# Optimization experiments

Measured on AMD Instinct MI355X. Metric: run time of the kernel, lower is better.

Reference implementation:

```python
import jax, jax.numpy as jnp
import numpy as np

B, S, E, H = 4, 2048, 1024, 16
DH = E // H  # 64
DF = 4 * E   # 4096
EPS = 1e-5


def layer_norm(x, g, b):
    mu = jnp.mean(x, axis=-1, keepdims=True)
    var = jnp.mean(jnp.square(x - mu), axis=-1, keepdims=True)
    return (x - mu) * jax.lax.rsqrt(var + EPS) * g + b


def setup_inputs() -> dict:
    key = jax.random.key(0)
    ks = jax.random.split(key, 16)
    s_e = 1.0 / np.sqrt(E)
    s_f = 1.0 / np.sqrt(DF)
    inp = {
        "x": jax.random.normal(ks[0], (B, S, E), jnp.float32),
        # per-head projections stacked over heads: [H, E, DH]
        "wq": jax.random.normal(ks[1], (H, E, DH), jnp.float32) * s_e,
        "wk": jax.random.normal(ks[2], (H, E, DH), jnp.float32) * s_e,
        "wv": jax.random.normal(ks[3], (H, E, DH), jnp.float32) * s_e,
        # output projection [H*DH, E] with bias
        "wo": jax.random.normal(ks[4], (H * DH, E), jnp.float32) * s_e,
        "bo": jax.random.normal(ks[5], (E,), jnp.float32) * 0.01,
        # SwiGLU FFN
        "w1": jax.random.normal(ks[6], (E, DF), jnp.float32) * s_e,
        "b1": jax.random.normal(ks[7], (DF,), jnp.float32) * 0.01,
        "w2": jax.random.normal(ks[8], (E, DF), jnp.float32) * s_e,
        "b2": jax.random.normal(ks[9], (DF,), jnp.float32) * 0.01,
        "w3": jax.random.normal(ks[10], (DF, E), jnp.float32) * s_f,
        "b3": jax.random.normal(ks[11], (E,), jnp.float32) * 0.01,
        # LayerNorm params
        "g1": jnp.ones((E,), jnp.float32),
        "be1": jnp.zeros((E,), jnp.float32),
        "g2": jnp.ones((E,), jnp.float32),
        "be2": jnp.zeros((E,), jnp.float32),
    }
    return inp


def reference(x, wq, wk, wv, wo, bo, w1, b1, w2, b2, w3, b3, g1, be1, g2, be2):
    # --- LN1 + multi-head causal attention ---
    h = layer_norm(x, g1, be1)                       # [B,S,E]
    q = jnp.einsum('bse,hed->bhsd', h, wq)           # [B,H,S,DH]
    k = jnp.einsum('bse,hed->bhsd', h, wk)
    v = jnp.einsum('bse,hed->bhsd', h, wv)
    scores = jnp.einsum('bhsd,bhtd->bhst', q, k) * (DH ** -0.5)  # [B,H,S,S]
    causal = jnp.tril(jnp.ones((S, S), bool))
    scores = jnp.where(causal, scores, -jnp.inf)
    attn = jax.nn.softmax(scores, axis=-1)
    ctx = jnp.einsum('bhst,bhtd->bhsd', attn, v)     # [B,H,S,DH]
    ctx = ctx.transpose(0, 2, 1, 3).reshape(B, S, H * DH)  # concat heads
    attn_out = ctx @ wo + bo                         # [B,S,E]
    r1 = x + attn_out
    # --- LN2 + SwiGLU FFN ---
    h2 = layer_norm(r1, g2, be2)
    a = h2 @ w1 + b1                                 # [B,S,DF]
    gate = h2 @ w2 + b2
    ff = (a * jax.nn.sigmoid(a) * gate) @ w3 + b3    # [B,S,E]
    return r1 + ff
```

## Files before the change

kernel.cpp:

```cpp
#include <hip/hip_runtime.h>
#include <hip/hip_bf16.h>
#include <cstdint>


typedef __bf16 bf16_t;
typedef __attribute__((ext_vector_type(8))) __bf16 bf16x8;
typedef __attribute__((ext_vector_type(4))) __bf16 bf16x4;
typedef __attribute__((ext_vector_type(4))) float f32x4;

#define LOG2E 1.4426950408889634f

static __device__ __forceinline__ void gll16(const void* g, void* l) {
  __builtin_amdgcn_global_load_lds(
      (const __attribute__((address_space(1))) void*)g,
      (__attribute__((address_space(3))) void*)l, 16, 0, 0);
}

__global__ __launch_bounds__(256)
void transpose_cvt(const float* __restrict__ in, bf16_t* __restrict__ out,
                   int R, int C, long in_batch, long out_batch)
{
  __shared__ float tile[64][65];
  const float* inp = in + (long)blockIdx.z * in_batch;
  bf16_t* outp = out + (long)blockIdx.z * out_batch;
  const int c0 = blockIdx.x * 64, r0 = blockIdx.y * 64;
  for (int rr = threadIdx.y; rr < 64; rr += 4)
    tile[rr][threadIdx.x] = inp[(long)(r0 + rr) * C + c0 + threadIdx.x];
  __syncthreads();
  for (int cc = threadIdx.y; cc < 64; cc += 4)
    outp[(long)(c0 + cc) * R + r0 + threadIdx.x] = (bf16_t)tile[threadIdx.x][cc];
}

__global__ __launch_bounds__(256)
void ln_kernel(const float* __restrict__ x, const float* __restrict__ g,
               const float* __restrict__ be, bf16_t* __restrict__ out)
{
  const long row = blockIdx.x;
  const float4 v = ((const float4*)(x + row * 1024))[threadIdx.x];
  float s  = v.x + v.y + v.z + v.w;
  float s2 = v.x*v.x + v.y*v.y + v.z*v.z + v.w*v.w;
  #pragma unroll
  for (int m = 1; m < 64; m <<= 1) {
    s  += __shfl_xor(s, m, 64);
    s2 += __shfl_xor(s2, m, 64);
  }
  __shared__ float red[8];
  const int w = threadIdx.x >> 6, lane = threadIdx.x & 63;
  if (lane == 0) { red[w] = s; red[4 + w] = s2; }
  __syncthreads();
  s  = red[0] + red[1] + red[2] + red[3];
  s2 = red[4] + red[5] + red[6] + red[7];
  const float mu = s * (1.f / 1024.f);
  const float rs = rsqrtf(s2 * (1.f / 1024.f) - mu * mu + 1e-5f);
  const int c = threadIdx.x * 4;
  bf16x4 o;
  o[0] = (bf16_t)((v.x - mu) * rs * g[c+0] + be[c+0]);
  o[1] = (bf16_t)((v.y - mu) * rs * g[c+1] + be[c+1]);
  o[2] = (bf16_t)((v.z - mu) * rs * g[c+2] + be[c+2]);
  o[3] = (bf16_t)((v.w - mu) * rs * g[c+3] + be[c+3]);
  *(bf16x4*)(out + row * 1024 + c) = o;
}

template<int EPI>
__global__ __launch_bounds__(256)
void gemm16(const bf16_t* __restrict__ A, const bf16_t* __restrict__ Bt,
            const float* __restrict__ bias, const float* __restrict__ res,
            float* __restrict__ outF,
            bf16_t* __restrict__ outQ, bf16_t* __restrict__ outK, bf16_t* __restrict__ outV,
            int M, int N, int K)
{
  __shared__ __align__(16) bf16_t As[2][128 * 32];
  __shared__ __align__(16) bf16_t Bs[2][128 * 32];
  const int tid = threadIdx.x, lane = tid & 63, w = tid >> 6;
  const int wr = w >> 1, wc = w & 1;
  const long row0 = (long)blockIdx.y * 128;
  const long col0 = (long)blockIdx.x * 128;
  const int rsub = lane >> 2;
  const int csub = (lane & 3) * 8;
  f32x4 acc[4][4] = {};

  auto stage = [&](long k0, int buf) {
    #pragma unroll
    for (int i = 0; i < 2; ++i) {
      const int c = i * 4 + w;
      gll16(A  + (row0 + c * 16 + rsub) * (long)K + k0 + csub, (char*)As[buf] + c * 1024);
      gll16(Bt + (col0 + c * 16 + rsub) * (long)K + k0 + csub, (char*)Bs[buf] + c * 1024);
    }
  };

  stage(0, 0);
  __syncthreads();
  int cur = 0;
  for (long k0 = 0; k0 < K; k0 += 32) {
    if (k0 + 32 < K) stage(k0 + 32, cur ^ 1);
    const int kof = (lane >> 4) * 8;
    bf16x8 af[4], bfr[4];
    #pragma unroll
    for (int m = 0; m < 4; ++m)
      af[m] = *(const bf16x8*)(As[cur] + (wr * 64 + m * 16 + (lane & 15)) * 32 + kof);
    #pragma unroll
    for (int n = 0; n < 4; ++n)
      bfr[n] = *(const bf16x8*)(Bs[cur] + (wc * 64 + n * 16 + (lane & 15)) * 32 + kof);
    #pragma unroll
    for (int m = 0; m < 4; ++m)
      #pragma unroll
      for (int n = 0; n < 4; ++n)
        acc[m][n] = __builtin_amdgcn_mfma_f32_16x16x32_bf16(af[m], bfr[n], acc[m][n], 0, 0, 0);
    __syncthreads();
    cur ^= 1;
  }
  #pragma unroll
  for (int m = 0; m < 4; ++m) {
    #pragma unroll
    for (int n = 0; n < 4; ++n) {
      const long cc = col0 + wc * 64 + n * 16 + (lane & 15);
      #pragma unroll
      for (int r = 0; r < 4; ++r) {
        const long rr = row0 + wr * 64 + m * 16 + (lane >> 4) * 4 + r;
        const float v = acc[m][n][r];
        if constexpr (EPI == 0) {
          const int which = (int)(cc >> 10);
          const int hh = (int)((cc >> 6) & 15);
          const int d  = (int)(cc & 63);
          const long b = rr >> 11, s = rr & 2047;
          const bf16_t bv = (bf16_t)v;
          const long bh = b * 16 + hh;
          if (which == 0)      outQ[(bh * 2048 + s) * 64 + d] = bv;
          else if (which == 1) outK[(bh * 2048 + s) * 64 + d] = bv;
          else                 outV[(bh * 64 + d) * 2048 + s] = bv;
        } else {
          outF[rr * N + cc] = v + bias[cc] + res[rr * N + cc];
        }
      }
    }
  }
}

__global__ __launch_bounds__(256)
void gemm_dual(const bf16_t* __restrict__ A,
               const bf16_t* __restrict__ B1t, const bf16_t* __restrict__ B2t,
               const float* __restrict__ bias1, const float* __restrict__ bias2,
               bf16_t* __restrict__ out, int M, int N, int K)
{
  __shared__ __align__(16) bf16_t As[2][128 * 32];
  __shared__ __align__(16) bf16_t B1s[2][64 * 32];
  __shared__ __align__(16) bf16_t B2s[2][64 * 32];
  const int tid = threadIdx.x, lane = tid & 63, w = tid >> 6;
  const int wr = w >> 1, wc = w & 1;
  const long row0 = (long)blockIdx.y * 128;
  const long col0 = (long)blockIdx.x * 64;
  const int rsub = lane >> 2;
  const int csub = (lane & 3) * 8;
  const int l15 = lane & 15;
  f32x4 acc1[4][2] = {}, acc2[4][2] = {};

  auto stage = [&](long k0, int buf) {
    gll16(A   + (row0 + w * 16       + rsub) * (long)K + k0 + csub, (char*)As[buf]  + w * 1024);
    gll16(A   + (row0 + (w + 4) * 16 + rsub) * (long)K + k0 + csub, (char*)As[buf]  + (w + 4) * 1024);
    gll16(B1t + (col0 + w * 16       + rsub) * (long)K + k0 + csub, (char*)B1s[buf] + w * 1024);
    gll16(B2t + (col0 + w * 16       + rsub) * (long)K + k0 + csub, (char*)B2s[buf] + w * 1024);
  };

  stage(0, 0);
  __syncthreads();
  int cur = 0;
  for (long k0 = 0; k0 < K; k0 += 32) {
    if (k0 + 32 < K) stage(k0 + 32, cur ^ 1);
    const int kof = (lane >> 4) * 8;
    bf16x8 af[4], b1f[2], b2f[2];
    #pragma unroll
    for (int m = 0; m < 4; ++m)
      af[m] = *(const bf16x8*)(As[cur] + (wr * 64 + m * 16 + l15) * 32 + kof);
    #pragma unroll
    for (int n = 0; n < 2; ++n) {
      b1f[n] = *(const bf16x8*)(B1s[cur] + (wc * 32 + n * 16 + l15) * 32 + kof);
      b2f[n] = *(const bf16x8*)(B2s[cur] + (wc * 32 + n * 16 + l15) * 32 + kof);
    }
    #pragma unroll
    for (int m = 0; m < 4; ++m)
      #pragma unroll
      for (int n = 0; n < 2; ++n) {
        acc1[m][n] = __builtin_amdgcn_mfma_f32_16x16x32_bf16(af[m], b1f[n], acc1[m][n], 0, 0, 0);
        acc2[m][n] = __builtin_amdgcn_mfma_f32_16x16x32_bf16(af[m], b2f[n], acc2[m][n], 0, 0, 0);
      }
    __syncthreads();
    cur ^= 1;
  }
  #pragma unroll
  for (int m = 0; m < 4; ++m) {
    #pragma unroll
    for (int n = 0; n < 2; ++n) {
      const long cc = col0 + wc * 32 + n * 16 + l15;
      #pragma unroll
      for (int r = 0; r < 4; ++r) {
        const long rr = row0 + wr * 64 + m * 16 + (lane >> 4) * 4 + r;
        const float a = acc1[m][n][r] + bias1[cc];
        const float gt = acc2[m][n][r] + bias2[cc];
        const float sig = 1.0f / (1.0f + __expf(-a));
        out[rr * N + cc] = (bf16_t)(a * sig * gt);
      }
    }
  }
}

__global__ __launch_bounds__(256, 4)
void attn_kernel(const bf16_t* __restrict__ q, const bf16_t* __restrict__ k,
                 const bf16_t* __restrict__ vT, bf16_t* __restrict__ ctx)
{
  __shared__ __align__(16) bf16_t Kb[2][64 * 64];
  __shared__ __align__(16) bf16_t Vb[2][64 * 64];
  __shared__ __align__(16) bf16_t plds[4][16 * 64];
  const int tid = threadIdx.x, lane = tid & 63, wvi = tid >> 6;
  const int bh = blockIdx.x;
  const bf16_t* qp = q  + (long)bh * 2048 * 64;
  const bf16_t* kp = k  + (long)bh * 2048 * 64;
  const bf16_t* vp = vT + (long)bh * 64 * 2048;
  const int l15 = lane & 15, lhi = lane >> 4;
  const long b = bh >> 4;
  const int hh = bh & 15;
  const int sw = (l15 & 7);
  const int psw = sw << 1;

  const int r0s = tid >> 3, cp0 = tid & 7, cl0 = cp0 ^ (r0s & 7);
  const int r1s = (tid + 256) >> 3, cp1 = tid & 7, cl1 = cp1 ^ (r1s & 7);

  #pragma unroll
  for (int seg = 0; seg < 2; ++seg) {
    const int ts = (seg == 0) ? blockIdx.y : 31 - blockIdx.y;
    const int qw0 = ts * 64 + wvi * 16;
    const int q_glob = qw0 + l15;
    bf16x8 qf[2];
    #pragma unroll
    for (int kk = 0; kk < 2; ++kk)
      qf[kk] = *(const bf16x8*)(qp + (long)(qw0 + l15) * 64 + kk * 32 + lhi * 8);
    f32x4 accO[4] = {};
    float mrow = -1e30f, lrow = 0.f;

    gll16(kp + (long)(0 + r0s) * 64 + cl0 * 8, (char*)Kb[0] + tid * 16);
    gll16(vp + (long)r0s * 2048 + 0 + cl0 * 8, (char*)Vb[0] + tid * 16);
    gll16(kp + (long)(0 + r1s) * 64 + cl1 * 8, (char*)Kb[0] + (tid + 256) * 16);
    gll16(vp + (long)r1s * 2048 + 0 + cl1 * 8, (char*)Vb[0] + (tid + 256) * 16);
    __syncthreads();

    int cur = 0;
    const int kbmax = ts * 64;
    for (int kb = 0; kb <= kbmax; kb += 64) {
      if (kb + 64 <= kbmax) {
        const int nb = kb + 64;
        gll16(kp + (long)(nb + r0s) * 64 + cl0 * 8, (char*)Kb[cur ^ 1] + tid * 16);
        gll16(vp + (long)r0s * 2048 + nb + cl0 * 8, (char*)Vb[cur ^ 1] + tid * 16);
        gll16(kp + (long)(nb + r1s) * 64 + cl1 * 8, (char*)Kb[cur ^ 1] + (tid + 256) * 16);
        gll16(vp + (long)r1s * 2048 + nb + cl1 * 8, (char*)Vb[cur ^ 1] + (tid + 256) * 16);
      }
      f32x4 accS[4] = {};
      #pragma unroll
      for (int n = 0; n < 4; ++n) {
        const bf16_t* kr = Kb[cur] + (n * 16 + l15) * 64;
        #pragma unroll
        for (int kk = 0; kk < 2; ++kk) {
          const bf16x8 kf = *(const bf16x8*)(kr + ((kk * 4 + lhi) ^ sw) * 8);
          accS[n] = __builtin_amdgcn_mfma_f32_16x16x32_bf16(kf, qf[kk], accS[n], 0, 0, 0);
        }
      }
      const bool needmask = (kb + 63 > qw0);
      float rmax = -1e30f;
      #pragma unroll
      for (int n = 0; n < 4; ++n)
        #pragma unroll
        for (int r = 0; r < 4; ++r) {
          float sv = accS[n][r] * 0.125f;
          if (needmask && (kb + n * 16 + lhi * 4 + r > q_glob)) sv = -1e30f;
          accS[n][r] = sv;
          rmax = fmaxf(rmax, sv);
        }
      rmax = fmaxf(rmax, __shfl_xor(rmax, 16, 64));
      rmax = fmaxf(rmax, __shfl_xor(rmax, 32, 64));
      const float mn = fmaxf(mrow, rmax);
      const float corr = exp2f((mrow - mn) * LOG2E);
      mrow = mn;
      float rsum = 0.f;
      #pragma unroll
      for (int n = 0; n < 4; ++n)
        #pragma unroll
        for (int r = 0; r < 4; ++r) {
          const float p = exp2f((accS[n][r] - mn) * LOG2E);
          accS[n][r] = p;
          rsum += p;
        }
      rsum += __shfl_xor(rsum, 16, 64);
      rsum += __shfl_xor(rsum, 32, 64);
      lrow = lrow * corr + rsum;
      #pragma unroll
      for (int nd = 0; nd < 4; ++nd)
        #pragma unroll
        for (int r = 0; r < 4; ++r) accO[nd][r] *= corr;
      #pragma unroll
      for (int n = 0; n < 4; ++n) {
        bf16x4 pk;
        #pragma unroll
        for (int r = 0; r < 4; ++r) pk[r] = (bf16_t)accS[n][r];
        *(bf16x4*)(&plds[wvi][l15 * 64 + ((4 * n + lhi) ^ psw) * 4]) = pk;
      }
      #pragma unroll
      for (int kk = 0; kk < 2; ++kk) {
        const bf16x8 pf = *(const bf16x8*)(&plds[wvi][l15 * 64 + ((8 * kk + 2 * lhi) ^ psw) * 4]);
        #pragma unroll
        for (int nd = 0; nd < 4; ++nd) {
          const bf16x8 vf = *(const bf16x8*)(Vb[cur] + (nd * 16 + l15) * 64 + ((kk * 4 + lhi) ^ sw) * 8);
          accO[nd] = __builtin_amdgcn_mfma_f32_16x16x32_bf16(vf, pf, accO[nd], 0, 0, 0);
        }
      }
      __syncthreads();
      cur ^= 1;
    }
    const float inv = 1.f / lrow;
    const long crow = (b * 2048 + qw0 + l15) * 1024 + hh * 64;
    #pragma unroll
    for (int nd = 0; nd < 4; ++nd) {
      bf16x4 ok;
      #pragma unroll
      for (int r = 0; r < 4; ++r) ok[r] = (bf16_t)(accO[nd][r] * inv);
      *(bf16x4*)(ctx + crow + nd * 16 + lhi * 4) = ok;
    }
  }
}

extern "C" void kernel_launch(void* const* d_in, const int* in_sizes, int n_in,
                              void* d_out, int out_size, void* d_ws, size_t ws_size,
                              hipStream_t stream)
{
  const float* x   = (const float*)d_in[0];
  const float* wq  = (const float*)d_in[1];
  const float* wk  = (const float*)d_in[2];
  const float* wv  = (const float*)d_in[3];
  const float* wo  = (const float*)d_in[4];
  const float* bo  = (const float*)d_in[5];
  const float* w1  = (const float*)d_in[6];
  const float* b1  = (const float*)d_in[7];
  const float* w2  = (const float*)d_in[8];
  const float* b2  = (const float*)d_in[9];
  const float* w3  = (const float*)d_in[10];
  const float* b3  = (const float*)d_in[11];
  const float* g1  = (const float*)d_in[12];
  const float* be1 = (const float*)d_in[13];
  const float* g2  = (const float*)d_in[14];
  const float* be2 = (const float*)d_in[15];
  float* out = (float*)d_out;

  char* ws = (char*)d_ws;
  bf16_t* h    = (bf16_t*)(ws);
  bf16_t* qb   = (bf16_t*)(ws + 16777216L);
  bf16_t* kb   = (bf16_t*)(ws + 2 * 16777216L);
  bf16_t* vTb  = (bf16_t*)(ws + 3 * 16777216L);
  float*  r1   = (float*)(ws + 4 * 16777216L);
  bf16_t* ffin = (bf16_t*)(ws + 4 * 16777216L + 33554432L);
  char* wbase  = ws + 4 * 16777216L + 33554432L + 67108864L;
  bf16_t* Wqkvt = (bf16_t*)(wbase);
  bf16_t* Wot   = (bf16_t*)(wbase + 6291456L);
  bf16_t* W1t   = (bf16_t*)(wbase + 8388608L);
  bf16_t* W2t   = (bf16_t*)(wbase + 16777216L);
  bf16_t* W3t   = (bf16_t*)(wbase + 25165824L);

  const dim3 tb(64, 4);
  transpose_cvt<<<dim3(1, 16, 16), tb, 0, stream>>>(wq, Wqkvt,            1024, 64, 65536, 65536);
  transpose_cvt<<<dim3(1, 16, 16), tb, 0, stream>>>(wk, Wqkvt + 1048576L, 1024, 64, 65536, 65536);
  transpose_cvt<<<dim3(1, 16, 16), tb, 0, stream>>>(wv, Wqkvt + 2097152L, 1024, 64, 65536, 65536);
  transpose_cvt<<<dim3(16, 16, 1), tb, 0, stream>>>(wo, Wot, 1024, 1024, 0, 0);
  transpose_cvt<<<dim3(64, 16, 1), tb, 0, stream>>>(w1, W1t, 1024, 4096, 0, 0);
  transpose_cvt<<<dim3(64, 16, 1), tb, 0, stream>>>(w2, W2t, 1024, 4096, 0, 0);
  transpose_cvt<<<dim3(16, 64, 1), tb, 0, stream>>>(w3, W3t, 4096, 1024, 0, 0);
  ln_kernel<<<8192, 256, 0, stream>>>(x, g1, be1, h);
  gemm16<0><<<dim3(24, 64), 256, 0, stream>>>(h, Wqkvt, nullptr, nullptr, nullptr,
                                              qb, kb, vTb, 8192, 3072, 1024);
  attn_kernel<<<dim3(64, 16), 256, 0, stream>>>(qb, kb, vTb, h);
  gemm16<1><<<dim3(8, 64), 256, 0, stream>>>(h, Wot, bo, x, r1,
                                             nullptr, nullptr, nullptr, 8192, 1024, 1024);
  ln_kernel<<<8192, 256, 0, stream>>>(r1, g2, be2, qb);
  gemm_dual<<<dim3(64, 64), 256, 0, stream>>>(qb, W1t, W2t, b1, b2, ffin, 8192, 4096, 1024);
  gemm16<1><<<dim3(8, 64), 256, 0, stream>>>(ffin, W3t, b3, r1, out,
                                             nullptr, nullptr, nullptr, 8192, 1024, 4096);
}
```

Baseline: 536.3 us.

## Triple-buffer GEMM LDS staging with partial vmcnt waits; add MFMA priority hints

```diff
diff --git a/kernel.cpp b/kernel.cpp
--- a/kernel.cpp
+++ b/kernel.cpp
@@ -14,6 +14,13 @@
   __builtin_amdgcn_global_load_lds(
       (const __attribute__((address_space(1))) void*)g,
       (__attribute__((address_space(3))) void*)l, 16, 0, 0);
+}
+
+static __device__ __forceinline__ void pipe_fence4() {
+  asm volatile("s_waitcnt vmcnt(4)" ::: "memory");
+  __builtin_amdgcn_sched_barrier(0);
+  __builtin_amdgcn_s_barrier();
+  __builtin_amdgcn_sched_barrier(0);
 }
 
 __global__ __launch_bounds__(256)
@@ -69,8 +76,8 @@
             bf16_t* __restrict__ outQ, bf16_t* __restrict__ outK, bf16_t* __restrict__ outV,
             int M, int N, int K)
 {
-  __shared__ __align__(16) bf16_t As[2][128 * 32];
-  __shared__ __align__(16) bf16_t Bs[2][128 * 32];
+  __shared__ __align__(16) bf16_t As[3][128 * 32];
+  __shared__ __align__(16) bf16_t Bs[3][128 * 32];
   const int tid = threadIdx.x, lane = tid & 63, w = tid >> 6;
   const int wr = w >> 1, wc = w & 1;
   const long row0 = (long)blockIdx.y * 128;
@@ -88,11 +95,18 @@
     }
   };
 
+  const int nsteps = K >> 5;
   stage(0, 0);
-  __syncthreads();
+  stage(nsteps > 1 ? 32 : 0, 1);
+  asm volatile("s_waitcnt vmcnt(4)" ::: "memory");
+  __builtin_amdgcn_sched_barrier(0);
+  __builtin_amdgcn_s_barrier();
+  __builtin_amdgcn_sched_barrier(0);
+
   int cur = 0;
-  for (long k0 = 0; k0 < K; k0 += 32) {
-    if (k0 + 32 < K) stage(k0 + 32, cur ^ 1);
+  for (int step = 0; step < nsteps; ++step) {
+    const long k2 = (long)((step + 2 < nsteps) ? step + 2 : nsteps - 1) * 32;
+    stage(k2, cur == 0 ? 2 : cur - 1);
     const int kof = (lane >> 4) * 8;
     bf16x8 af[4], bfr[4];
     #pragma unroll
@@ -106,9 +120,11 @@
       #pragma unroll
       for (int n = 0; n < 4; ++n)
         acc[m][n] = __builtin_amdgcn_mfma_f32_16x16x32_bf16(af[m], bfr[n], acc[m][n], 0, 0, 0);
-    __syncthreads();
-    cur ^= 1;
-  }
+    pipe_fence4();
+    cur = (cur == 2) ? 0 : cur + 1;
+  }
+  asm volatile("s_waitcnt vmcnt(0)" ::: "memory");
+
   #pragma unroll
   for (int m = 0; m < 4; ++m) {
     #pragma unroll
@@ -142,9 +158,9 @@
                const float* __restrict__ bias1, const float* __restrict__ bias2,
                bf16_t* __restrict__ out, int M, int N, int K)
 {
-  __shared__ __align__(16) bf16_t As[2][128 * 32];
-  __shared__ __align__(16) bf16_t B1s[2][64 * 32];
-  __shared__ __align__(16) bf16_t B2s[2][64 * 32];
+  __shared__ __align__(16) bf16_t As[3][128 * 32];
+  __shared__ __align__(16) bf16_t B1s[3][64 * 32];
+  __shared__ __align__(16) bf16_t B2s[3][64 * 32];
   const int tid = threadIdx.x, lane = tid & 63, w = tid >> 6;
   const int wr = w >> 1, wc = w & 1;
   const long row0 = (long)blockIdx.y * 128;
@@ -161,11 +177,18 @@
     gll16(B2t + (col0 + w * 16       + rsub) * (long)K + k0 + csub, (char*)B2s[buf] + w * 1024);
   };
 
+  const int nsteps = K >> 5;
   stage(0, 0);
-  __syncthreads();
+  stage(nsteps > 1 ? 32 : 0, 1);
+  asm volatile("s_waitcnt vmcnt(4)" ::: "memory");
+  __builtin_amdgcn_sched_barrier(0);
+  __builtin_amdgcn_s_barrier();
+  __builtin_amdgcn_sched_barrier(0);
+
   int cur = 0;
-  for (long k0 = 0; k0 < K; k0 += 32) {
-    if (k0 + 32 < K) stage(k0 + 32, cur ^ 1);
+  for (int step = 0; step < nsteps; ++step) {
+    const long k2 = (long)((step + 2 < nsteps) ? step + 2 : nsteps - 1) * 32;
+    stage(k2, cur == 0 ? 2 : cur - 1);
     const int kof = (lane >> 4) * 8;
     bf16x8 af[4], b1f[2], b2f[2];
     #pragma unroll
@@ -183,9 +206,11 @@
         acc1[m][n] = __builtin_amdgcn_mfma_f32_16x16x32_bf16(af[m], b1f[n], acc1[m][n], 0, 0, 0);
         acc2[m][n] = __builtin_amdgcn_mfma_f32_16x16x32_bf16(af[m], b2f[n], acc2[m][n], 0, 0, 0);
       }
-    __syncthreads();
-    cur ^= 1;
-  }
+    pipe_fence4();
+    cur = (cur == 2) ? 0 : cur + 1;
+  }
+  asm volatile("s_waitcnt vmcnt(0)" ::: "memory");
+
   #pragma unroll
   for (int m = 0; m < 4; ++m) {
     #pragma unroll
@@ -253,6 +278,7 @@
         gll16(vp + (long)r1s * 2048 + nb + cl1 * 8, (char*)Vb[cur ^ 1] + (tid + 256) * 16);
       }
       f32x4 accS[4] = {};
+      __builtin_amdgcn_s_setprio(1);
       #pragma unroll
       for (int n = 0; n < 4; ++n) {
         const bf16_t* kr = Kb[cur] + (n * 16 + l15) * 64;
@@ -262,6 +288,7 @@
           accS[n] = __builtin_amdgcn_mfma_f32_16x16x32_bf16(kf, qf[kk], accS[n], 0, 0, 0);
         }
       }
+      __builtin_amdgcn_s_setprio(0);
       const bool needmask = (kb + 63 > qw0);
       float rmax = -1e30f;
       #pragma unroll
@@ -301,6 +328,7 @@
         for (int r = 0; r < 4; ++r) pk[r] = (bf16_t)accS[n][r];
         *(bf16x4*)(&plds[wvi][l15 * 64 + ((4 * n + lhi) ^ psw) * 4]) = pk;
       }
+      __builtin_amdgcn_s_setprio(1);
       #pragma unroll
       for (int kk = 0; kk < 2; ++kk) {
         const bf16x8 pf = *(const bf16x8*)(&plds[wvi][l15 * 64 + ((8 * kk + 2 * lhi) ^ psw) * 4]);
@@ -310,6 +338,7 @@
           accO[nd] = __builtin_amdgcn_mfma_f32_16x16x32_bf16(vf, pf, accO[nd], 0, 0, 0);
         }
       }
+      __builtin_amdgcn_s_setprio(0);
       __syncthreads();
       cur ^= 1;
     }
```

New measurement: 579.8 us. 1.08x slower.
